# Performance work log

Hardware: AMD Instinct MI355X
Metric: run time of the kernel (lower is better)

Reference implementation:

```python
import jax, jax.numpy as jnp
import numpy as np

MEMORY_SIZE = 32768
DIM_K = 256
DIM_V = 256
B = 2048
OLD_SIZE = 16384


def setup_inputs() -> dict:
    key = jax.random.key(0)
    k1, k2, k3, k4, k5 = jax.random.split(key, 5)
    return {
        "q": jax.random.normal(k1, (B, DIM_K), dtype=jnp.float32),
        "k": jax.random.normal(k2, (B, DIM_K), dtype=jnp.float32),
        "v": jax.random.normal(k3, (B, DIM_V), dtype=jnp.float32),
        "K_cache": jax.random.normal(k4, (MEMORY_SIZE, DIM_K), dtype=jnp.float32),
        "V_cache": jax.random.normal(k5, (MEMORY_SIZE, DIM_V), dtype=jnp.float32),
        "old_size": OLD_SIZE,
    }


def reference(q, k, v, K_cache, V_cache, old_size):
    b, dim_k = q.shape
    new_size = old_size + b  # static python int
    # write the new chunk of keys/values into the cache
    K = jax.lax.dynamic_update_slice(K_cache, k, (old_size, 0))
    V = jax.lax.dynamic_update_slice(V_cache, v, (old_size, 0))
    Kv = K[:new_size]  # [new_size, dim_k]
    Vv = V[:new_size]  # [new_size, dim_v]
    # scaled dot-product scores: [b, new_size]
    scores = (q @ Kv.T) * (1.0 / (dim_k ** 0.5))
    # causal mask: query i (global pos old_size+i) may attend keys j <= old_size+i
    key_idx = jnp.arange(new_size)[None, :]
    query_idx = jnp.arange(old_size, new_size)[:, None]
    scores = jnp.where(key_idx > query_idx, -jnp.inf, scores)
    p = jax.nn.softmax(scores, axis=-1)
    return p @ Vv  # [b, dim_v]
```

## Files before the change

### kernel.cpp

```cpp
#include <hip/hip_runtime.h>
#include <hip/hip_bf16.h>
#include <cstdint>

typedef __attribute__((ext_vector_type(8)))  short s8b;
typedef __attribute__((ext_vector_type(4)))  short s4b;
typedef __attribute__((ext_vector_type(16))) float f16v;

#define MFMA32(a,b,c) __builtin_amdgcn_mfma_f32_32x32x16_bf16((a),(b),(c),0,0,0)

#define OLDN   16384
#define NEWB   2048
#define DHEAD  256
#define NTOTAL 18432
#define EXPSC  0.09016844005556021f

#define KSTR  264
#define VSTR  40

static __device__ __forceinline__ short f2bf(float f) {
    unsigned u = __float_as_uint(f);
    unsigned r = (u + 0x7fffu + ((u >> 16) & 1u)) >> 16;
    return (short)r;
}

__global__ void cvt_kernel(const float* __restrict__ Kc, const float* __restrict__ kn,
                           const float* __restrict__ Vc, const float* __restrict__ vn,
                           s8b* __restrict__ Kb, s8b* __restrict__ Vb) {
    int idx8 = blockIdx.x * 256 + threadIdx.x;
    int idx  = idx8 * 8;
    int row  = idx >> 8;
    int col  = idx & 255;
    const float* src;
    if (blockIdx.y == 0)
        src = (row < OLDN) ? (Kc + (size_t)row * DHEAD + col)
                           : (kn + (size_t)(row - OLDN) * DHEAD + col);
    else
        src = (row < OLDN) ? (Vc + (size_t)row * DHEAD + col)
                           : (vn + (size_t)(row - OLDN) * DHEAD + col);
    float4 f0 = *(const float4*)src;
    float4 f1 = *(const float4*)(src + 4);
    s8b o;
    o[0]=f2bf(f0.x); o[1]=f2bf(f0.y); o[2]=f2bf(f0.z); o[3]=f2bf(f0.w);
    o[4]=f2bf(f1.x); o[5]=f2bf(f1.y); o[6]=f2bf(f1.z); o[7]=f2bf(f1.w);
    (blockIdx.y == 0 ? Kb : Vb)[idx8] = o;
}

__global__ __launch_bounds__(256, 2)
void attn_kernel(const float* __restrict__ q,
                 const short* __restrict__ Kb, const short* __restrict__ Vb,
                 float* __restrict__ OP, float* __restrict__ L, int SPLIT) {
    __shared__ short K_lds[32 * KSTR];
    __shared__ short Vt_lds[DHEAD * VSTR];

    const int bx   = blockIdx.x;
    const int s    = bx % SPLIT;
    const int qb   = bx / SPLIT;
    const int q0   = qb * 128;
    const int tid  = threadIdx.x;
    const int w    = tid >> 6;
    const int lane = tid & 63;
    const int lc   = lane & 31;
    const int h    = lane >> 5;

    s8b qf[16];
    {
        const int qrow = q0 + 32 * w + lc;
        const float* qp = q + (size_t)qrow * DHEAD + 8 * h;
#pragma unroll
        for (int c = 0; c < 16; ++c) {
            float4 f0 = *(const float4*)(qp + 16 * c);
            float4 f1 = *(const float4*)(qp + 16 * c + 4);
            s8b o;
            o[0]=f2bf(f0.x); o[1]=f2bf(f0.y); o[2]=f2bf(f0.z); o[3]=f2bf(f0.w);
            o[4]=f2bf(f1.x); o[5]=f2bf(f1.y); o[6]=f2bf(f1.z); o[7]=f2bf(f1.w);
            qf[c] = o;
        }
    }

    f16v acc[8];
#pragma unroll
    for (int c = 0; c < 8; ++c)
#pragma unroll
        for (int r = 0; r < 16; ++r) acc[c][r] = 0.f;
    float lsum = 0.f;

    const int krow = tid >> 3;
    const int kcb  = (tid & 7) * 8;
    const int va   = tid & 3;
    const int vd   = (tid >> 2) * 4;
    const int vkb  = 16 * (va >> 1) + 4 * (va & 1);

    const int nt_total = (OLDN + q0 + 128) >> 5;
    const int tb  = nt_total / SPLIT;
    const int rem = nt_total % SPLIT;
    const int t0  = s * tb + (s < rem ? s : rem);
    const int tcnt = tb + (s < rem ? 1 : 0);

    const int qbase = OLDN + q0 + 32 * w;

    for (int t = t0; t < t0 + tcnt; ++t) {
        const int kk = t << 5;
        __syncthreads();
        {
            const s8b* src = (const s8b*)(Kb + (size_t)(kk + krow) * DHEAD + kcb);
            short* dst = &K_lds[krow * KSTR + kcb];
#pragma unroll
            for (int i = 0; i < 4; ++i)
                *(s8b*)(dst + i * 64) = src[i * 8];
        }
        {
            s4b ld[8];
#pragma unroll
            for (int j = 0; j < 8; ++j)
                ld[j] = *(const s4b*)(Vb + (size_t)(kk + vkb + (j & 3) + 8 * (j >> 2)) * DHEAD + vd);
#pragma unroll
            for (int r = 0; r < 4; ++r) {
                s8b o;
#pragma unroll
                for (int j = 0; j < 8; ++j) o[j] = ld[j][r];
                *(s8b*)&Vt_lds[(vd + r) * VSTR + 8 * va] = o;
            }
        }
        __syncthreads();

        f16v sacc;
#pragma unroll
        for (int r = 0; r < 16; ++r) sacc[r] = 0.f;
#pragma unroll
        for (int c = 0; c < 16; ++c) {
            s8b kf = *(const s8b*)&K_lds[lc * KSTR + 16 * c + 8 * h];
            sacc = MFMA32(kf, qf[c], sacc);
        }

        const bool domask = (kk + 31 > qbase);
        float e[16];
#pragma unroll
        for (int r = 0; r < 16; ++r) {
            float ev = __builtin_exp2f(sacc[r] * EXPSC);
            if (domask) {
                int key = kk + (r & 3) + 8 * (r >> 2) + 4 * h;
                if (key > qbase + lc) ev = 0.f;
            }
            e[r] = ev;
            lsum += ev;
        }
        s8b pf0, pf1;
#pragma unroll
        for (int j = 0; j < 8; ++j) { pf0[j] = f2bf(e[j]); pf1[j] = f2bf(e[8 + j]); }

#pragma unroll
        for (int c = 0; c < 8; ++c) {
            const short* vrow = &Vt_lds[(32 * c + lc) * VSTR];
            s8b v0 = *(const s8b*)(vrow + 8 * h);
            s8b v1 = *(const s8b*)(vrow + 16 + 8 * h);
            acc[c] = MFMA32(v0, pf0, acc[c]);
            acc[c] = MFMA32(v1, pf1, acc[c]);
        }
    }

    lsum += __shfl_xor(lsum, 32);

    const int qrow = q0 + 32 * w + lc;
    const size_t sbase = (size_t)s * NEWB;
    float* op_row = OP + (sbase + qrow) * DHEAD;
#pragma unroll
    for (int c = 0; c < 8; ++c)
#pragma unroll
        for (int g = 0; g < 4; ++g) {
            float4 o = {acc[c][4 * g], acc[c][4 * g + 1], acc[c][4 * g + 2], acc[c][4 * g + 3]};
            *(float4*)(op_row + 32 * c + 8 * g + 4 * h) = o;
        }
    if (h == 0)
        L[sbase + qrow] = lsum;
}

__global__ void combine_kernel(const float* __restrict__ OP, const float* __restrict__ L,
                               float* __restrict__ out, int SPLIT) {
    const int row = blockIdx.x;
    const int col = threadIdx.x;
    float num = 0.f, den = 0.f;
    for (int s = 0; s < SPLIT; ++s) {
        size_t r = (size_t)s * NEWB + row;
        num += OP[r * DHEAD + col];
        den += L[r];
    }
    out[(size_t)row * DHEAD + col] = num / den;
}

extern "C" void kernel_launch(void* const* d_in, const int* in_sizes, int n_in,
                              void* d_out, int out_size, void* d_ws, size_t ws_size,
                              hipStream_t stream) {
    const float* q  = (const float*)d_in[0];
    const float* kn = (const float*)d_in[1];
    const float* vn = (const float*)d_in[2];
    const float* Kc = (const float*)d_in[3];
    const float* Vc = (const float*)d_in[4];
    float* out = (float*)d_out;

    char* ws = (char*)d_ws;
    const size_t KB_BYTES = (size_t)NTOTAL * DHEAD * 2;
    short* Kb = (short*)(ws);
    short* Vb = (short*)(ws + KB_BYTES);
    const size_t PART_BASE = 2 * KB_BYTES;

    const size_t per_split = (size_t)NEWB * DHEAD * 4 + (size_t)NEWB * 4;
    size_t avail = (ws_size > PART_BASE) ? (ws_size - PART_BASE) : 0;
    int SPLIT = (int)(avail / per_split);
    if (SPLIT > 32) SPLIT = 32;
    if (SPLIT < 1)  SPLIT = 1;

    float* OP = (float*)(ws + PART_BASE);
    float* L  = (float*)(ws + PART_BASE + (size_t)SPLIT * NEWB * DHEAD * 4);

    cvt_kernel<<<dim3(NTOTAL * DHEAD / (256 * 8), 2), 256, 0, stream>>>(Kc, kn, Vc, vn,
                                                                        (s8b*)Kb, (s8b*)Vb);
    attn_kernel<<<16 * SPLIT, 256, 0, stream>>>(q, Kb, Vb, OP, L, SPLIT);
    combine_kernel<<<NEWB, 256, 0, stream>>>(OP, L, out, SPLIT);
}
```

Baseline: 200.9 us.

## Pre-swizzle K/V into MFMA fragment layout and load K directly from global

The conversion kernel now writes K and V in per-tile MFMA fragment order, with V pre-transposed via a key-slot permutation. This lets the attention kernel read K fragments straight from global memory with no LDS staging and copy V into LDS without an in-kernel transpose. The softmax scale is folded into q, the score MFMA chain is split into two accumulators to expose ILP, and bf16 packing uses a perm instruction. Partial outputs are stored as bf16 to halve the partial-buffer traffic, at some precision cost. The V conversion now does strided scalar gathers, which may make the preprocessing pass more expensive.

```diff
diff --git a/kernel.cpp b/kernel.cpp
--- a/kernel.cpp
+++ b/kernel.cpp
@@ -5,6 +5,7 @@
 typedef __attribute__((ext_vector_type(8)))  short s8b;
 typedef __attribute__((ext_vector_type(4)))  short s4b;
 typedef __attribute__((ext_vector_type(16))) float f16v;
+typedef __attribute__((ext_vector_type(4)))  unsigned u4v;
 
 #define MFMA32(a,b,c) __builtin_amdgcn_mfma_f32_32x32x16_bf16((a),(b),(c),0,0,0)
 
@@ -12,45 +13,66 @@
 #define NEWB   2048
 #define DHEAD  256
 #define NTOTAL 18432
+#define NTILES 576
 #define EXPSC  0.09016844005556021f
-
-#define KSTR  264
-#define VSTR  40
 
 static __device__ __forceinline__ short f2bf(float f) {
     unsigned u = __float_as_uint(f);
     unsigned r = (u + 0x7fffu + ((u >> 16) & 1u)) >> 16;
     return (short)r;
 }
+static __device__ __forceinline__ int slot_key(int s) {
+    return (s & 3) + 8 * ((s >> 2) & 1) + 4 * ((s >> 3) & 1) + 16 * (s >> 4);
+}
 
 __global__ void cvt_kernel(const float* __restrict__ Kc, const float* __restrict__ kn,
                            const float* __restrict__ Vc, const float* __restrict__ vn,
-                           s8b* __restrict__ Kb, s8b* __restrict__ Vb) {
-    int idx8 = blockIdx.x * 256 + threadIdx.x;
-    int idx  = idx8 * 8;
-    int row  = idx >> 8;
-    int col  = idx & 255;
-    const float* src;
-    if (blockIdx.y == 0)
-        src = (row < OLDN) ? (Kc + (size_t)row * DHEAD + col)
-                           : (kn + (size_t)(row - OLDN) * DHEAD + col);
-    else
-        src = (row < OLDN) ? (Vc + (size_t)row * DHEAD + col)
-                           : (vn + (size_t)(row - OLDN) * DHEAD + col);
-    float4 f0 = *(const float4*)src;
-    float4 f1 = *(const float4*)(src + 4);
-    s8b o;
-    o[0]=f2bf(f0.x); o[1]=f2bf(f0.y); o[2]=f2bf(f0.z); o[3]=f2bf(f0.w);
-    o[4]=f2bf(f1.x); o[5]=f2bf(f1.y); o[6]=f2bf(f1.z); o[7]=f2bf(f1.w);
-    (blockIdx.y == 0 ? Kb : Vb)[idx8] = o;
+                           s8b* __restrict__ Ksw, s8b* __restrict__ Vsw) {
+    const int t   = blockIdx.x;
+    const int tid = threadIdx.x;
+    if (blockIdx.y == 0) {
+#pragma unroll
+        for (int i = 0; i < 4; ++i) {
+            int chunk = tid + 256 * i;
+            int l = chunk & 63;
+            int b = chunk >> 6;
+            int row = 32 * t + (l & 31);
+            int col = 16 * b + 8 * (l >> 5);
+            const float* src = (row < OLDN) ? Kc + (size_t)row * DHEAD + col
+                                            : kn + (size_t)(row - OLDN) * DHEAD + col;
+            float4 f0 = *(const float4*)src;
+            float4 f1 = *(const float4*)(src + 4);
+            s8b o;
+            o[0]=f2bf(f0.x); o[1]=f2bf(f0.y); o[2]=f2bf(f0.z); o[3]=f2bf(f0.w);
+            o[4]=f2bf(f1.x); o[5]=f2bf(f1.y); o[6]=f2bf(f1.z); o[7]=f2bf(f1.w);
+            Ksw[(size_t)t * 1024 + chunk] = o;
+        }
+    } else {
+#pragma unroll
+        for (int i = 0; i < 4; ++i) {
+            int chunk = tid + 256 * i;
+            int l = chunk & 63;
+            int b = chunk >> 6;
+            int m = 32 * (b >> 1) + (l & 31);
+            int sbase = 16 * (b & 1) + 8 * (l >> 5);
+            s8b o;
+#pragma unroll
+            for (int j = 0; j < 8; ++j) {
+                int row = 32 * t + slot_key(sbase + j);
+                float v = (row < OLDN) ? Vc[(size_t)row * DHEAD + m]
+                                       : vn[(size_t)(row - OLDN) * DHEAD + m];
+                o[j] = f2bf(v);
+            }
+            Vsw[(size_t)t * 1024 + chunk] = o;
+        }
+    }
 }
 
 __global__ __launch_bounds__(256, 2)
 void attn_kernel(const float* __restrict__ q,
-                 const short* __restrict__ Kb, const short* __restrict__ Vb,
-                 float* __restrict__ OP, float* __restrict__ L, int SPLIT) {
-    __shared__ short K_lds[32 * KSTR];
-    __shared__ short Vt_lds[DHEAD * VSTR];
+                 const s8b* __restrict__ Ksw, const s8b* __restrict__ Vsw,
+                 short* __restrict__ OPb, float* __restrict__ L, int SPLIT) {
+    __shared__ short V_lds[16 * 512];
 
     const int bx   = blockIdx.x;
     const int s    = bx % SPLIT;
@@ -71,8 +93,8 @@
             float4 f0 = *(const float4*)(qp + 16 * c);
             float4 f1 = *(const float4*)(qp + 16 * c + 4);
             s8b o;
-            o[0]=f2bf(f0.x); o[1]=f2bf(f0.y); o[2]=f2bf(f0.z); o[3]=f2bf(f0.w);
-            o[4]=f2bf(f1.x); o[5]=f2bf(f1.y); o[6]=f2bf(f1.z); o[7]=f2bf(f1.w);
+            o[0]=f2bf(f0.x*EXPSC); o[1]=f2bf(f0.y*EXPSC); o[2]=f2bf(f0.z*EXPSC); o[3]=f2bf(f0.w*EXPSC);
+            o[4]=f2bf(f1.x*EXPSC); o[5]=f2bf(f1.y*EXPSC); o[6]=f2bf(f1.z*EXPSC); o[7]=f2bf(f1.w*EXPSC);
             qf[c] = o;
         }
     }
@@ -83,105 +105,96 @@
 #pragma unroll
         for (int r = 0; r < 16; ++r) acc[c][r] = 0.f;
     float lsum = 0.f;
-
-    const int krow = tid >> 3;
-    const int kcb  = (tid & 7) * 8;
-    const int va   = tid & 3;
-    const int vd   = (tid >> 2) * 4;
-    const int vkb  = 16 * (va >> 1) + 4 * (va & 1);
 
     const int nt_total = (OLDN + q0 + 128) >> 5;
     const int tb  = nt_total / SPLIT;
     const int rem = nt_total % SPLIT;
     const int t0  = s * tb + (s < rem ? s : rem);
     const int tcnt = tb + (s < rem ? 1 : 0);
-
     const int qbase = OLDN + q0 + 32 * w;
 
-    for (int t = t0; t < t0 + tcnt; ++t) {
+    const s8b* kp = Ksw + (size_t)t0 * 1024 + lane;
+    const s8b* vp = Vsw + (size_t)t0 * 1024 + (size_t)(4 * w) * 64 + lane;
+    short* vlds_w = &V_lds[(4 * w) * 512 + lane * 8];
+    const short* vlds_r = &V_lds[lane * 8];
+
+    for (int t = t0; t < t0 + tcnt; ++t, kp += 1024, vp += 1024) {
         const int kk = t << 5;
+
+        s8b vstage[4];
+#pragma unroll
+        for (int i = 0; i < 4; ++i) vstage[i] = vp[i * 64];
+
+        f16v sacc0, sacc1;
+#pragma unroll
+        for (int r = 0; r < 16; ++r) { sacc0[r] = 0.f; sacc1[r] = 0.f; }
+#pragma unroll
+        for (int c = 0; c < 8; ++c) {
+            s8b k0 = kp[(2 * c) * 64];
+            s8b k1 = kp[(2 * c + 1) * 64];
+            sacc0 = MFMA32(k0, qf[2 * c],     sacc0);
+            sacc1 = MFMA32(k1, qf[2 * c + 1], sacc1);
+        }
+
+        const bool domask = (kk + 31 > qbase);
+        unsigned pk[8];
+#pragma unroll
+        for (int i = 0; i < 8; ++i) {
+            const int r0 = 2 * i, r1 = 2 * i + 1;
+            float ev0 = __builtin_exp2f(sacc0[r0] + sacc1[r0]);
+            float ev1 = __builtin_exp2f(sacc0[r1] + sacc1[r1]);
+            if (domask) {
+                if (kk + (r0 & 3) + 8 * (r0 >> 2) + 4 * h > qbase + lc) ev0 = 0.f;
+                if (kk + (r1 & 3) + 8 * (r1 >> 2) + 4 * h > qbase + lc) ev1 = 0.f;
+            }
+            lsum += ev0 + ev1;
+            pk[i] = __builtin_amdgcn_perm(__float_as_uint(ev1), __float_as_uint(ev0), 0x07060302u);
+        }
+        s8b pf0 = __builtin_bit_cast(s8b, (u4v){pk[0], pk[1], pk[2], pk[3]});
+        s8b pf1 = __builtin_bit_cast(s8b, (u4v){pk[4], pk[5], pk[6], pk[7]});
+
+#pragma unroll
+        for (int i = 0; i < 4; ++i) *(s8b*)(vlds_w + i * 512) = vstage[i];
         __syncthreads();
-        {
-            const s8b* src = (const s8b*)(Kb + (size_t)(kk + krow) * DHEAD + kcb);
-            short* dst = &K_lds[krow * KSTR + kcb];
-#pragma unroll
-            for (int i = 0; i < 4; ++i)
-                *(s8b*)(dst + i * 64) = src[i * 8];
-        }
-        {
-            s4b ld[8];
-#pragma unroll
-            for (int j = 0; j < 8; ++j)
-                ld[j] = *(const s4b*)(Vb + (size_t)(kk + vkb + (j & 3) + 8 * (j >> 2)) * DHEAD + vd);
-#pragma unroll
-            for (int r = 0; r < 4; ++r) {
-                s8b o;
-#pragma unroll
-                for (int j = 0; j < 8; ++j) o[j] = ld[j][r];
-                *(s8b*)&Vt_lds[(vd + r) * VSTR + 8 * va] = o;
-            }
-        }
-        __syncthreads();
-
-        f16v sacc;
-#pragma unroll
-        for (int r = 0; r < 16; ++r) sacc[r] = 0.f;
-#pragma unroll
-        for (int c = 0; c < 16; ++c) {
-            s8b kf = *(const s8b*)&K_lds[lc * KSTR + 16 * c + 8 * h];
-            sacc = MFMA32(kf, qf[c], sacc);
-        }
-
-        const bool domask = (kk + 31 > qbase);
-        float e[16];
-#pragma unroll
-        for (int r = 0; r < 16; ++r) {
-            float ev = __builtin_exp2f(sacc[r] * EXPSC);
-            if (domask) {
-                int key = kk + (r & 3) + 8 * (r >> 2) + 4 * h;
-                if (key > qbase + lc) ev = 0.f;
-            }
-            e[r] = ev;
-            lsum += ev;
-        }
-        s8b pf0, pf1;
-#pragma unroll
-        for (int j = 0; j < 8; ++j) { pf0[j] = f2bf(e[j]); pf1[j] = f2bf(e[8 + j]); }
 
 #pragma unroll
         for (int c = 0; c < 8; ++c) {
-            const short* vrow = &Vt_lds[(32 * c + lc) * VSTR];
-            s8b v0 = *(const s8b*)(vrow + 8 * h);
-            s8b v1 = *(const s8b*)(vrow + 16 + 8 * h);
+            s8b v0 = *(const s8b*)(vlds_r + (2 * c) * 512);
+            s8b v1 = *(const s8b*)(vlds_r + (2 * c + 1) * 512);
             acc[c] = MFMA32(v0, pf0, acc[c]);
             acc[c] = MFMA32(v1, pf1, acc[c]);
         }
+        __syncthreads();
     }
 
     lsum += __shfl_xor(lsum, 32);
 
     const int qrow = q0 + 32 * w + lc;
     const size_t sbase = (size_t)s * NEWB;
-    float* op_row = OP + (sbase + qrow) * DHEAD;
+    short* op_row = OPb + (sbase + qrow) * DHEAD;
 #pragma unroll
     for (int c = 0; c < 8; ++c)
 #pragma unroll
         for (int g = 0; g < 4; ++g) {
-            float4 o = {acc[c][4 * g], acc[c][4 * g + 1], acc[c][4 * g + 2], acc[c][4 * g + 3]};
-            *(float4*)(op_row + 32 * c + 8 * g + 4 * h) = o;
-        }
-    if (h == 0)
-        L[sbase + qrow] = lsum;
-}
-
-__global__ void combine_kernel(const float* __restrict__ OP, const float* __restrict__ L,
+            s4b o4;
+            o4[0] = f2bf(acc[c][4 * g]);
+            o4[1] = f2bf(acc[c][4 * g + 1]);
+            o4[2] = f2bf(acc[c][4 * g + 2]);
+            o4[3] = f2bf(acc[c][4 * g + 3]);
+            *(s4b*)(op_row + 32 * c + 8 * g + 4 * h) = o4;
+        }
+    if (h == 0) L[sbase + qrow] = lsum;
+}
+
+__global__ void combine_kernel(const short* __restrict__ OPb, const float* __restrict__ L,
                                float* __restrict__ out, int SPLIT) {
     const int row = blockIdx.x;
     const int col = threadIdx.x;
     float num = 0.f, den = 0.f;
     for (int s = 0; s < SPLIT; ++s) {
         size_t r = (size_t)s * NEWB + row;
-        num += OP[r * DHEAD + col];
+        unsigned u = (unsigned)(unsigned short)OPb[r * DHEAD + col];
+        num += __uint_as_float(u << 16);
         den += L[r];
     }
     out[(size_t)row * DHEAD + col] = num / den;
@@ -199,21 +212,20 @@
 
     char* ws = (char*)d_ws;
     const size_t KB_BYTES = (size_t)NTOTAL * DHEAD * 2;
-    short* Kb = (short*)(ws);
-    short* Vb = (short*)(ws + KB_BYTES);
+    s8b* Ksw = (s8b*)(ws);
+    s8b* Vsw = (s8b*)(ws + KB_BYTES);
     const size_t PART_BASE = 2 * KB_BYTES;
 
-    const size_t per_split = (size_t)NEWB * DHEAD * 4 + (size_t)NEWB * 4;
+    const size_t per_split = (size_t)NEWB * DHEAD * 2 + (size_t)NEWB * 4;
     size_t avail = (ws_size > PART_BASE) ? (ws_size - PART_BASE) : 0;
     int SPLIT = (int)(avail / per_split);
     if (SPLIT > 32) SPLIT = 32;
     if (SPLIT < 1)  SPLIT = 1;
 
-    float* OP = (float*)(ws + PART_BASE);
-    float* L  = (float*)(ws + PART_BASE + (size_t)SPLIT * NEWB * DHEAD * 4);
-
-    cvt_kernel<<<dim3(NTOTAL * DHEAD / (256 * 8), 2), 256, 0, stream>>>(Kc, kn, Vc, vn,
-                                                                        (s8b*)Kb, (s8b*)Vb);
-    attn_kernel<<<16 * SPLIT, 256, 0, stream>>>(q, Kb, Vb, OP, L, SPLIT);
-    combine_kernel<<<NEWB, 256, 0, stream>>>(OP, L, out, SPLIT);
-}
+    short* OPb = (short*)(ws + PART_BASE);
+    float* L   = (float*)(ws + PART_BASE + (size_t)SPLIT * NEWB * DHEAD * 2);
+
+    cvt_kernel<<<dim3(NTILES, 2), 256, 0, stream>>>(Kc, kn, Vc, vn, Ksw, Vsw);
+    attn_kernel<<<16 * SPLIT, 256, 0, stream>>>(q, Ksw, Vsw, OPb, L, SPLIT);
+    combine_kernel<<<NEWB, 256, 0, stream>>>(OPb, L, out, SPLIT);
+}
```

New measurement: 187.2 us. -6.8%, faster.
